# Kernel tuning notes

Measured on AMD Instinct MI355X. Metric: run time of the kernel, lower is better.

Reference implementation:

```python
import jax, jax.numpy as jnp
import numpy as np

B = 8
S_MAX = 1024
H = 12
HD = 64
D = H * HD
DFF = 4 * D
NEG = -1.0e9  # matches Triton kernel's -1000000000.0 mask value


def _layernorm(x, g, b, eps=1e-6):
    mu = jnp.mean(x, axis=-1, keepdims=True)
    var = jnp.mean((x - mu) ** 2, axis=-1, keepdims=True)
    return (x - mu) * jax.lax.rsqrt(var + eps) * g + b


def setup_inputs() -> dict:
    key = jax.random.key(0)
    ks = jax.random.split(key, 12)
    lengths = np.array([1024, 896, 768, 640, 896, 1024, 512, 384], dtype=np.int32)
    assert lengths.max() <= S_MAX and len(lengths) == B
    total = int(lengths.sum())  # 6144
    cu = jnp.asarray(np.concatenate([[0], np.cumsum(lengths)]), dtype=jnp.int32)
    s = 0.02
    return {
        "x": jax.random.normal(ks[0], (total, D), jnp.float32),
        "cu_seqlens": cu,
        "g1": jnp.ones((D,), jnp.float32),
        "beta1": jnp.zeros((D,), jnp.float32),
        "Wqkv": jax.random.normal(ks[1], (D, 3 * D), jnp.float32) * s,
        "bqkv": jnp.zeros((3 * D,), jnp.float32),
        "Wo": jax.random.normal(ks[2], (D, D), jnp.float32) * s,
        "bo": jnp.zeros((D,), jnp.float32),
        "g2": jnp.ones((D,), jnp.float32),
        "beta2": jnp.zeros((D,), jnp.float32),
        "W1": jax.random.normal(ks[3], (D, DFF), jnp.float32) * s,
        "b_fc1": jnp.zeros((DFF,), jnp.float32),
        "W2": jax.random.normal(ks[4], (DFF, D), jnp.float32) * s,
        "b_fc2": jnp.zeros((D,), jnp.float32),
    }


def _ragged_attention(q, k, v, cu_seqlens):
    # q,k,v: [Total, H, HD] packed ragged sequences; cu_seqlens: [B+1] int32
    total = q.shape[0]
    lens = cu_seqlens[1:] - cu_seqlens[:-1]                      # [B]
    s = jnp.arange(S_MAX)
    pad_idx = cu_seqlens[:-1, None] + jnp.minimum(s[None, :], lens[:, None] - 1)  # [B,S]
    valid = s[None, :] < lens[:, None]                           # [B,S]
    qp = q[pad_idx]                                              # [B,S,H,HD]
    kp = k[pad_idx]
    vp = v[pad_idx]
    scale = 1.0 / jnp.sqrt(jnp.float32(HD))
    scores = jnp.einsum("bqhd,bkhd->bhqk", qp, kp) * scale      # [B,H,S,S]
    scores = jnp.where(valid[:, None, None, :], scores, NEG)     # mask invalid keys
    p = jax.nn.softmax(scores, axis=-1)
    op = jnp.einsum("bhqk,bkhd->bqhd", p, vp)                   # [B,S,H,HD]
    # repack to [Total, H, HD]
    tok = jnp.arange(total)
    seg = jnp.searchsorted(cu_seqlens, tok, side="right") - 1    # sequence id per token
    pos = tok - cu_seqlens[seg]
    return op[seg, pos]


def _forward(x, cu_seqlens, g1, beta1, Wqkv, bqkv, Wo, bo, g2, beta2, W1, b_fc1, W2, b_fc2):
    total = x.shape[0]
    qkv = (_layernorm(x, g1, beta1) @ Wqkv + bqkv).reshape(total, 3, H, HD)
    q, k, v = qkv[:, 0], qkv[:, 1], qkv[:, 2]
    attn = _ragged_attention(q, k, v, cu_seqlens).reshape(total, D)
    x = x + (attn @ Wo + bo)                                     # proj_drop/ls1/drop_path identity (eval)
    h = _layernorm(x, g2, beta2)
    m = jax.nn.gelu(h @ W1 + b_fc1, approximate=False)
    return x + (m @ W2 + b_fc2)


def reference(x, cu_seqlens, g1, beta1, Wqkv, bqkv, Wo, bo, g2, beta2, W1, b_fc1, W2, b_fc2):
    return _forward(x, cu_seqlens, g1, beta1, Wqkv, bqkv, Wo, bo, g2, beta2, W1, b_fc1, W2, b_fc2)
```

## Files before the change

### kernel.cpp

```cpp
#include <hip/hip_runtime.h>
#include <hip/hip_bf16.h>
#include <stdint.h>
#include <string.h>

#define D_MODEL 768
#define H_HEADS 12
#define HD_ 64
#define N_QKV 2304

typedef __bf16 bf16x8 __attribute__((ext_vector_type(8)));
typedef float f32x4 __attribute__((ext_vector_type(4)));

__device__ __forceinline__ unsigned short f2bfbits(float f) {
  union { float f; unsigned u; } x; x.f = f;
  unsigned r = x.u + 0x7fffu + ((x.u >> 16) & 1u);
  return (unsigned short)(r >> 16);
}

__device__ __forceinline__ unsigned pk2(float a, float b) {
  union { float f; unsigned u; } x, y; x.f = a; y.f = b;
  return ((x.u + 0x8000u) >> 16) | ((y.u + 0x8000u) & 0xffff0000u);
}

#define FENCE_() __builtin_amdgcn_sched_barrier(0)
__device__ __forceinline__ void store_sync() {
  FENCE_();
  asm volatile("s_waitcnt lgkmcnt(0)");
  FENCE_();
  __builtin_amdgcn_s_barrier();
  FENCE_();
}

__global__ void transpose_w(const float* __restrict__ in, unsigned short* __restrict__ out,
                            int R, int C) {
  __shared__ float tile[32][33];
  int c0 = blockIdx.x * 32, r0 = blockIdx.y * 32;
  int tx = threadIdx.x, ty = threadIdx.y;
#pragma unroll
  for (int i = 0; i < 32; i += 8)
    tile[ty + i][tx] = in[(size_t)(r0 + ty + i) * C + c0 + tx];
  __syncthreads();
#pragma unroll
  for (int i = 0; i < 32; i += 8)
    out[(size_t)(c0 + ty + i) * R + r0 + tx] = f2bfbits(tile[tx][ty + i]);
}

__global__ void transpose_v(const unsigned short* __restrict__ qkv,
                            unsigned short* __restrict__ vT, int M) {
  __shared__ unsigned short tile[32][33];
  int t0 = blockIdx.x * 32, c0 = blockIdx.y * 32;
  int tx = threadIdx.x, ty = threadIdx.y;
#pragma unroll
  for (int i = 0; i < 32; i += 8)
    tile[ty + i][tx] = qkv[(size_t)(t0 + ty + i) * N_QKV + 1536 + c0 + tx];
  __syncthreads();
  int t = t0 + tx;
  int c = t & 63;
  int kp = ((c >> 5) << 5) | (((c >> 2) & 3) << 3) | (((c >> 4) & 1) << 2) | (c & 3);
  size_t col = (size_t)(t & ~63) + kp;
#pragma unroll
  for (int i = 0; i < 32; i += 8)
    vT[(size_t)(c0 + ty + i) * M + col] = tile[tx][ty + i];
}

__global__ void ln_bf16(const float* __restrict__ x, const float* __restrict__ g,
                        const float* __restrict__ be, unsigned short* __restrict__ out) {
  int row = blockIdx.x;
  const float* xr = x + (size_t)row * D_MODEL;
  int t = threadIdx.x;
  float v0 = xr[t], v1 = xr[t + 256], v2 = xr[t + 512];
  float s = v0 + v1 + v2;
  float s2 = v0 * v0 + v1 * v1 + v2 * v2;
#pragma unroll
  for (int off = 32; off > 0; off >>= 1) {
    s += __shfl_down(s, off, 64);
    s2 += __shfl_down(s2, off, 64);
  }
  __shared__ float red[8];
  int w = t >> 6, lane = t & 63;
  if (lane == 0) { red[w] = s; red[w + 4] = s2; }
  __syncthreads();
  if (t == 0) {
    float a = red[0] + red[1] + red[2] + red[3];
    float b = red[4] + red[5] + red[6] + red[7];
    red[0] = a * (1.0f / 768.0f);
    red[4] = b * (1.0f / 768.0f);
  }
  __syncthreads();
  float mu = red[0];
  float var = red[4] - mu * mu;
  float rs = rsqrtf(var + 1e-6f);
  unsigned short* orow = out + (size_t)row * D_MODEL;
  orow[t]       = f2bfbits((v0 - mu) * rs * g[t]       + be[t]);
  orow[t + 256] = f2bfbits((v1 - mu) * rs * g[t + 256] + be[t + 256]);
  orow[t + 512] = f2bfbits((v2 - mu) * rs * g[t + 512] + be[t + 512]);
}

template <int EPI>
__global__ void __launch_bounds__(256, 3)
gemm_rs(const unsigned short* __restrict__ A,
        const unsigned short* __restrict__ Bt,
        const float* __restrict__ bias,
        const float* __restrict__ res,
        void* __restrict__ outv,
        int M, int N, int K) {
  __shared__ unsigned short lA[2][128 * 32];
  __shared__ unsigned short lB[2][128 * 32];
  int tid = threadIdx.x;
  int w = tid >> 6, lane = tid & 63;
  int id = blockIdx.x;
  int nn = N >> 7, bandM = (M >> 7) >> 3;
  int xcd = id & 7, s = id >> 3;
  int mt = xcd * bandM + s / nn;
  int nt = s - (s / nn) * nn;
  int m0 = mt * 128, n0 = nt * 128;
  int wm = (w >> 1) * 64, wn = (w & 1) * 64;
  f32x4 acc[4][4];
#pragma unroll
  for (int i = 0; i < 4; i++)
#pragma unroll
    for (int j = 0; j < 4; j++) acc[i][j] = (f32x4){0.f, 0.f, 0.f, 0.f};

  int sr = tid >> 2, sc = tid & 3;
  const unsigned short* gA = A + (size_t)(m0 + sr) * K + sc * 8;
  const unsigned short* gB = Bt + (size_t)(n0 + sr) * K + sc * 8;
  int wOff = sr * 64 + ((((sr >> 1) & 3) ^ sc) * 16);
  int fm = lane & 15, fg = lane >> 4;

  uint4 pA0, pA1, pB0, pB1;
  uint4 qA0, qA1, qB0, qB1;

  int nk = K >> 5;
  pA0 = *(const uint4*)(gA);
  pA1 = *(const uint4*)(gA + (size_t)64 * K);
  pB0 = *(const uint4*)(gB);
  pB1 = *(const uint4*)(gB + (size_t)64 * K);
  qA0 = *(const uint4*)(gA + 32);
  qA1 = *(const uint4*)(gA + (size_t)64 * K + 32);
  qB0 = *(const uint4*)(gB + 32);
  qB1 = *(const uint4*)(gB + (size_t)64 * K + 32);

  for (int k = 0; k < nk; k += 2) {
    {
      char* la = (char*)&lA[0][0];
      char* lb = (char*)&lB[0][0];
      *(uint4*)(la + wOff) = pA0;
      *(uint4*)(la + wOff + 4096) = pA1;
      *(uint4*)(lb + wOff) = pB0;
      *(uint4*)(lb + wOff + 4096) = pB1;
      if (k + 2 < nk) {
        int k0 = (k + 2) * 32;
        pA0 = *(const uint4*)(gA + k0);
        pA1 = *(const uint4*)(gA + (size_t)64 * K + k0);
        pB0 = *(const uint4*)(gB + k0);
        pB1 = *(const uint4*)(gB + (size_t)64 * K + k0);
      }
      store_sync();
      bf16x8 af[4], bfr[4];
#pragma unroll
      for (int i = 0; i < 4; i++) {
        int rr = wm + i * 16 + fm;
        af[i] = *(const bf16x8*)(la + rr * 64 + ((((rr >> 1) & 3) ^ fg) * 16));
      }
#pragma unroll
      for (int j = 0; j < 4; j++) {
        int rr = wn + j * 16 + fm;
        bfr[j] = *(const bf16x8*)(lb + rr * 64 + ((((rr >> 1) & 3) ^ fg) * 16));
      }
#pragma unroll
      for (int i = 0; i < 4; i++)
#pragma unroll
        for (int j = 0; j < 4; j++)
          acc[i][j] = __builtin_amdgcn_mfma_f32_16x16x32_bf16(af[i], bfr[j], acc[i][j], 0, 0, 0);
      store_sync();
    }
    {
      char* la = (char*)&lA[1][0];
      char* lb = (char*)&lB[1][0];
      *(uint4*)(la + wOff) = qA0;
      *(uint4*)(la + wOff + 4096) = qA1;
      *(uint4*)(lb + wOff) = qB0;
      *(uint4*)(lb + wOff + 4096) = qB1;
      if (k + 3 < nk) {
        int k0 = (k + 3) * 32;
        qA0 = *(const uint4*)(gA + k0);
        qA1 = *(const uint4*)(gA + (size_t)64 * K + k0);
        qB0 = *(const uint4*)(gB + k0);
        qB1 = *(const uint4*)(gB + (size_t)64 * K + k0);
      }
      store_sync();
      bf16x8 af[4], bfr[4];
#pragma unroll
      for (int i = 0; i < 4; i++) {
        int rr = wm + i * 16 + fm;
        af[i] = *(const bf16x8*)(la + rr * 64 + ((((rr >> 1) & 3) ^ fg) * 16));
      }
#pragma unroll
      for (int j = 0; j < 4; j++) {
        int rr = wn + j * 16 + fm;
        bfr[j] = *(const bf16x8*)(lb + rr * 64 + ((((rr >> 1) & 3) ^ fg) * 16));
      }
#pragma unroll
      for (int i = 0; i < 4; i++)
#pragma unroll
        for (int j = 0; j < 4; j++)
          acc[i][j] = __builtin_amdgcn_mfma_f32_16x16x32_bf16(af[i], bfr[j], acc[i][j], 0, 0, 0);
      store_sync();
    }
  }

  int er = (lane >> 4) * 4, ec = lane & 15;
#pragma unroll
  for (int i = 0; i < 4; i++) {
#pragma unroll
    for (int j = 0; j < 4; j++) {
      int n = n0 + wn + j * 16 + ec;
      float bv = bias[n];
#pragma unroll
      for (int r = 0; r < 4; r++) {
        int m = m0 + wm + i * 16 + er + r;
        float v = acc[i][j][r] + bv;
        if (EPI == 1) {
          v += res[(size_t)m * N + n];
          ((float*)outv)[(size_t)m * N + n] = v;
        } else {
          if (EPI == 2) v = 0.5f * v * (1.0f + erff(v * 0.70710678118f));
          ((unsigned short*)outv)[(size_t)m * N + n] = f2bfbits(v);
        }
      }
    }
  }
}

template <int EPI>
__global__ void __launch_bounds__(256, 4)
gemm_n64(const unsigned short* __restrict__ A,
         const unsigned short* __restrict__ Bt,
         const float* __restrict__ bias,
         const float* __restrict__ res,
         void* __restrict__ outv,
         int M, int N, int K) {
  __shared__ unsigned short lA[2][128 * 32];
  __shared__ unsigned short lB[2][64 * 32];
  int tid = threadIdx.x;
  int w = tid >> 6, lane = tid & 63;
  int id = blockIdx.x;
  int nn = N >> 6, bandM = (M >> 7) >> 3;
  int xcd = id & 7, s = id >> 3;
  int mt = xcd * bandM + s / nn;
  int nt = s - (s / nn) * nn;
  int m0 = mt * 128, n0 = nt * 64;
  int wm = w * 32;
  f32x4 acc[2][4];
#pragma unroll
  for (int i = 0; i < 2; i++)
#pragma unroll
    for (int j = 0; j < 4; j++) acc[i][j] = (f32x4){0.f, 0.f, 0.f, 0.f};

  int sr = tid >> 2, sc = tid & 3;
  const unsigned short* gA = A + (size_t)(m0 + sr) * K + sc * 8;
  const unsigned short* gB = Bt + (size_t)(n0 + sr) * K + sc * 8;
  int wOff = sr * 64 + ((((sr >> 1) & 3) ^ sc) * 16);
  int fm = lane & 15, fg = lane >> 4;

  uint4 pA0, pA1, pB0;
  uint4 qA0, qA1, qB0;

  int nk = K >> 5;
  pA0 = *(const uint4*)(gA);
  pA1 = *(const uint4*)(gA + (size_t)64 * K);
  pB0 = *(const uint4*)(gB);
  qA0 = *(const uint4*)(gA + 32);
  qA1 = *(const uint4*)(gA + (size_t)64 * K + 32);
  qB0 = *(const uint4*)(gB + 32);

  for (int k = 0; k < nk; k += 2) {
    {
      char* la = (char*)&lA[0][0];
      char* lb = (char*)&lB[0][0];
      *(uint4*)(la + wOff) = pA0;
      *(uint4*)(la + wOff + 4096) = pA1;
      *(uint4*)(lb + wOff) = pB0;
      if (k + 2 < nk) {
        int k0 = (k + 2) * 32;
        pA0 = *(const uint4*)(gA + k0);
        pA1 = *(const uint4*)(gA + (size_t)64 * K + k0);
        pB0 = *(const uint4*)(gB + k0);
      }
      store_sync();
      bf16x8 af[2], bfr[4];
#pragma unroll
      for (int i = 0; i < 2; i++) {
        int rr = wm + i * 16 + fm;
        af[i] = *(const bf16x8*)(la + rr * 64 + ((((rr >> 1) & 3) ^ fg) * 16));
      }
#pragma unroll
      for (int j = 0; j < 4; j++) {
        int rr = j * 16 + fm;
        bfr[j] = *(const bf16x8*)(lb + rr * 64 + ((((rr >> 1) & 3) ^ fg) * 16));
      }
#pragma unroll
      for (int i = 0; i < 2; i++)
#pragma unroll
        for (int j = 0; j < 4; j++)
          acc[i][j] = __builtin_amdgcn_mfma_f32_16x16x32_bf16(af[i], bfr[j], acc[i][j], 0, 0, 0);
      store_sync();
    }
    {
      char* la = (char*)&lA[1][0];
      char* lb = (char*)&lB[1][0];
      *(uint4*)(la + wOff) = qA0;
      *(uint4*)(la + wOff + 4096) = qA1;
      *(uint4*)(lb + wOff) = qB0;
      if (k + 3 < nk) {
        int k0 = (k + 3) * 32;
        qA0 = *(const uint4*)(gA + k0);
        qA1 = *(const uint4*)(gA + (size_t)64 * K + k0);
        qB0 = *(const uint4*)(gB + k0);
      }
      store_sync();
      bf16x8 af[2], bfr[4];
#pragma unroll
      for (int i = 0; i < 2; i++) {
        int rr = wm + i * 16 + fm;
        af[i] = *(const bf16x8*)(la + rr * 64 + ((((rr >> 1) & 3) ^ fg) * 16));
      }
#pragma unroll
      for (int j = 0; j < 4; j++) {
        int rr = j * 16 + fm;
        bfr[j] = *(const bf16x8*)(lb + rr * 64 + ((((rr >> 1) & 3) ^ fg) * 16));
      }
#pragma unroll
      for (int i = 0; i < 2; i++)
#pragma unroll
        for (int j = 0; j < 4; j++)
          acc[i][j] = __builtin_amdgcn_mfma_f32_16x16x32_bf16(af[i], bfr[j], acc[i][j], 0, 0, 0);
      store_sync();
    }
  }

  int er = (lane >> 4) * 4, ec = lane & 15;
#pragma unroll
  for (int i = 0; i < 2; i++) {
#pragma unroll
    for (int j = 0; j < 4; j++) {
      int n = n0 + j * 16 + ec;
      float bv = bias[n];
#pragma unroll
      for (int r = 0; r < 4; r++) {
        int m = m0 + wm + i * 16 + er + r;
        float v = acc[i][j][r] + bv;
        if (EPI == 1) {
          v += res[(size_t)m * N + n];
          ((float*)outv)[(size_t)m * N + n] = v;
        } else {
          if (EPI == 2) v = 0.5f * v * (1.0f + erff(v * 0.70710678118f));
          ((unsigned short*)outv)[(size_t)m * N + n] = f2bfbits(v);
        }
      }
    }
  }
}

__global__ void attn_flash4(const unsigned short* __restrict__ qkv,
                            const unsigned short* __restrict__ vT,
                            const int* __restrict__ cu,
                            unsigned short* __restrict__ out, int M) {
  int id = blockIdx.x;
  int qc = id / 96;
  int bh = id - qc * 96;
  int b = bh / 12, h = bh - b * 12;
  int tok0 = cu[b];
  int len = cu[b + 1] - tok0;
  if (qc * 128 >= len) return;

  __shared__ unsigned short lK[2][64 * 64];
  __shared__ unsigned short lVT[2][64 * 64];

  int tid = threadIdx.x, w = tid >> 6, lane = tid & 63;
  int fm = lane & 15, fg = lane >> 4;
  int xm = fm & 7;
  int qbase = qc * 128 + w * 32;

  bf16x8 qf[2][2];
#pragma unroll
  for (int qs = 0; qs < 2; qs++)
#pragma unroll
    for (int kh = 0; kh < 2; kh++)
      qf[qs][kh] = *(const bf16x8*)(qkv + (size_t)(tok0 + qbase + qs * 16 + fm) * N_QKV +
                                    h * 64 + kh * 32 + fg * 8);

  f32x4 Oacc[2][4];
#pragma unroll
  for (int qs = 0; qs < 2; qs++)
#pragma unroll
    for (int dt = 0; dt < 4; dt++) Oacc[qs][dt] = (f32x4){0.f, 0.f, 0.f, 0.f};
  float lrow[2] = {0.f, 0.f};
  const float C2 = 0.18033688011112042f;

  int sr = tid >> 3, sp = tid & 7, sl = sp ^ (sr & 7);
  const unsigned short* kg0 = qkv + D_MODEL + h * 64 + sl * 8;
  const unsigned short* vg0 = vT + (size_t)(h * 64 + sr) * M + tok0 + sl * 8;

  uint4 rk0, rk1, rv0, rv1;
  auto gload = [&](int kt) {
    rk0 = *(const uint4*)(kg0 + (size_t)(tok0 + kt + sr) * N_QKV);
    rk1 = *(const uint4*)(kg0 + (size_t)(tok0 + kt + sr + 32) * N_QKV);
    rv0 = *(const uint4*)(vg0 + kt);
    rv1 = *(const uint4*)(vg0 + (size_t)32 * M + kt);
  };

  int nkt = len >> 6;
  gload(0);
  for (int kt = 0; kt < nkt; kt++) {
    int cur = kt & 1;
    *(uint4*)((char*)&lK[cur][0] + tid * 16) = rk0;
    *(uint4*)((char*)&lK[cur][0] + tid * 16 + 4096) = rk1;
    *(uint4*)((char*)&lVT[cur][0] + tid * 16) = rv0;
    *(uint4*)((char*)&lVT[cur][0] + tid * 16 + 4096) = rv1;
    if (kt + 1 < nkt) gload((kt + 1) * 64);
    store_sync();

    f32x4 s[2][4];
#pragma unroll
    for (int qs = 0; qs < 2; qs++)
#pragma unroll
      for (int t = 0; t < 4; t++) s[qs][t] = (f32x4){0.f, 0.f, 0.f, 0.f};
#pragma unroll
    for (int t = 0; t < 4; t++) {
      bf16x8 kf0 = *(const bf16x8*)&lK[cur][(t * 16 + fm) * 64 + ((fg ^ xm) * 8)];
      bf16x8 kf1 = *(const bf16x8*)&lK[cur][(t * 16 + fm) * 64 + (((4 + fg) ^ xm) * 8)];
#pragma unroll
      for (int qs = 0; qs < 2; qs++) {
        s[qs][t] = __builtin_amdgcn_mfma_f32_16x16x32_bf16(kf0, qf[qs][0], s[qs][t], 0, 0, 0);
        s[qs][t] = __builtin_amdgcn_mfma_f32_16x16x32_bf16(kf1, qf[qs][1], s[qs][t], 0, 0, 0);
      }
    }

    union { bf16x8 v; unsigned u[4]; } af[2][2];
#pragma unroll
    for (int qs = 0; qs < 2; qs++) {
      float ssum = 0.f;
#pragma unroll
      for (int t = 0; t < 4; t++) {
#pragma unroll
        for (int r = 0; r < 4; r++) {
          float p = exp2f(s[qs][t][r] * C2);
          s[qs][t][r] = p;
          ssum += p;
        }
      }
      lrow[qs] += ssum;
      af[qs][0].u[0] = pk2(s[qs][0][0], s[qs][0][1]);
      af[qs][0].u[1] = pk2(s[qs][0][2], s[qs][0][3]);
      af[qs][0].u[2] = pk2(s[qs][1][0], s[qs][1][1]);
      af[qs][0].u[3] = pk2(s[qs][1][2], s[qs][1][3]);
      af[qs][1].u[0] = pk2(s[qs][2][0], s[qs][2][1]);
      af[qs][1].u[1] = pk2(s[qs][2][2], s[qs][2][3]);
      af[qs][1].u[2] = pk2(s[qs][3][0], s[qs][3][1]);
      af[qs][1].u[3] = pk2(s[qs][3][2], s[qs][3][3]);
    }

#pragma unroll
    for (int dt = 0; dt < 4; dt++) {
      bf16x8 vf0 = *(const bf16x8*)&lVT[cur][(dt * 16 + fm) * 64 + ((fg ^ xm) * 8)];
      bf16x8 vf1 = *(const bf16x8*)&lVT[cur][(dt * 16 + fm) * 64 + (((4 + fg) ^ xm) * 8)];
#pragma unroll
      for (int qs = 0; qs < 2; qs++) {
        Oacc[qs][dt] = __builtin_amdgcn_mfma_f32_16x16x32_bf16(af[qs][0].v, vf0, Oacc[qs][dt], 0, 0, 0);
        Oacc[qs][dt] = __builtin_amdgcn_mfma_f32_16x16x32_bf16(af[qs][1].v, vf1, Oacc[qs][dt], 0, 0, 0);
      }
    }
  }

#pragma unroll
  for (int qs = 0; qs < 2; qs++) {
    lrow[qs] += __shfl_xor(lrow[qs], 16, 64);
    lrow[qs] += __shfl_xor(lrow[qs], 32, 64);
    float inv = 1.0f / lrow[qs];
    float ir[4];
#pragma unroll
    for (int r = 0; r < 4; r++) ir[r] = __shfl(inv, fg * 4 + r, 64);
#pragma unroll
    for (int dt = 0; dt < 4; dt++)
#pragma unroll
      for (int r = 0; r < 4; r++)
        out[(size_t)(tok0 + qbase + qs * 16 + fg * 4 + r) * D_MODEL + h * 64 + dt * 16 + fm] =
            f2bfbits(Oacc[qs][dt][r] * ir[r]);
  }
}

extern "C" void kernel_launch(void* const* d_in, const int* in_sizes, int n_in,
                              void* d_out, int out_size, void* d_ws, size_t ws_size,
                              hipStream_t stream) {
  const float* x    = (const float*)d_in[0];
  const int* cu     = (const int*)d_in[1];
  const float* g1   = (const float*)d_in[2];
  const float* be1  = (const float*)d_in[3];
  const float* Wqkv = (const float*)d_in[4];
  const float* bqkv = (const float*)d_in[5];
  const float* Wo   = (const float*)d_in[6];
  const float* bo   = (const float*)d_in[7];
  const float* g2   = (const float*)d_in[8];
  const float* be2  = (const float*)d_in[9];
  const float* W1   = (const float*)d_in[10];
  const float* bfc1 = (const float*)d_in[11];
  const float* W2   = (const float*)d_in[12];
  const float* bfc2 = (const float*)d_in[13];
  float* out = (float*)d_out;
  int M = in_sizes[0] / D_MODEL;

  unsigned short* WqkvT = (unsigned short*)d_ws;
  unsigned short* WoT   = WqkvT + 2304 * 768;
  unsigned short* W1T   = WoT + 768 * 768;
  unsigned short* W2T   = W1T + 3072 * 768;
  unsigned short* bufA  = W2T + 768 * 3072;
  float* x1             = (float*)(bufA + (size_t)M * D_MODEL);
  unsigned short* qkvb  = (unsigned short*)(x1 + (size_t)M * D_MODEL);
  unsigned short* vT = (unsigned short*)x1;

  dim3 b32(32, 8);
  transpose_w<<<dim3(2304 / 32, 768 / 32), b32, 0, stream>>>(Wqkv, WqkvT, 768, 2304);
  transpose_w<<<dim3(768 / 32, 768 / 32), b32, 0, stream>>>(Wo, WoT, 768, 768);
  transpose_w<<<dim3(3072 / 32, 768 / 32), b32, 0, stream>>>(W1, W1T, 768, 3072);
  transpose_w<<<dim3(768 / 32, 3072 / 32), b32, 0, stream>>>(W2, W2T, 3072, 768);

  ln_bf16<<<M, 256, 0, stream>>>(x, g1, be1, bufA);
  gemm_rs<0><<<(2304 / 128) * (M / 128), 256, 0, stream>>>(bufA, WqkvT, bqkv, nullptr, qkvb, M, 2304, 768);
  transpose_v<<<dim3(M / 32, 768 / 32), b32, 0, stream>>>(qkvb, vT, M);
  attn_flash4<<<8 * 96, 256, 0, stream>>>(qkvb, vT, cu, bufA, M);
  gemm_n64<1><<<(768 / 64) * (M / 128), 256, 0, stream>>>(bufA, WoT, bo, x, x1, M, 768, 768);
  ln_bf16<<<M, 256, 0, stream>>>(x1, g2, be2, bufA);
  gemm_rs<2><<<(3072 / 128) * (M / 128), 256, 0, stream>>>(bufA, W1T, bfc1, nullptr, qkvb, M, 3072, 768);
  gemm_n64<1><<<(768 / 64) * (M / 128), 256, 0, stream>>>(qkvb, W2T, bfc2, x1, out, M, 768, 3072);
}
```

Before: 343.3 us.

## Load GEMM A fragments directly from global memory, bypassing LDS staging

Both GEMM kernels now read the A-operand MFMA fragments straight from global memory into registers instead of staging A through double-buffered shared memory. Only B is staged in LDS, and the trailing barrier of each half-step is dropped because the double-buffered B tiles stay race-free with one barrier per stage. The aim is to cut LDS traffic, LDS footprint and barrier count. In exchange, A loads are issued in the same stage they are consumed with no register prefetch, so global-load latency may be exposed. Waves sharing the same A rows also fetch them redundantly from cache.

```diff
diff --git a/kernel.cpp b/kernel.cpp
--- a/kernel.cpp
+++ b/kernel.cpp
@@ -104,7 +104,6 @@
         const float* __restrict__ res,
         void* __restrict__ outv,
         int M, int N, int K) {
-  __shared__ unsigned short lA[2][128 * 32];
   __shared__ unsigned short lB[2][128 * 32];
   int tid = threadIdx.x;
   int w = tid >> 6, lane = tid & 63;
@@ -122,46 +121,34 @@
     for (int j = 0; j < 4; j++) acc[i][j] = (f32x4){0.f, 0.f, 0.f, 0.f};
 
   int sr = tid >> 2, sc = tid & 3;
-  const unsigned short* gA = A + (size_t)(m0 + sr) * K + sc * 8;
   const unsigned short* gB = Bt + (size_t)(n0 + sr) * K + sc * 8;
   int wOff = sr * 64 + ((((sr >> 1) & 3) ^ sc) * 16);
   int fm = lane & 15, fg = lane >> 4;
-
-  uint4 pA0, pA1, pB0, pB1;
-  uint4 qA0, qA1, qB0, qB1;
-
+  const unsigned short* gAf = A + (size_t)(m0 + wm + fm) * K + fg * 8;
+
+  uint4 pB0, pB1, qB0, qB1;
   int nk = K >> 5;
-  pA0 = *(const uint4*)(gA);
-  pA1 = *(const uint4*)(gA + (size_t)64 * K);
   pB0 = *(const uint4*)(gB);
   pB1 = *(const uint4*)(gB + (size_t)64 * K);
-  qA0 = *(const uint4*)(gA + 32);
-  qA1 = *(const uint4*)(gA + (size_t)64 * K + 32);
   qB0 = *(const uint4*)(gB + 32);
   qB1 = *(const uint4*)(gB + (size_t)64 * K + 32);
 
   for (int k = 0; k < nk; k += 2) {
     {
-      char* la = (char*)&lA[0][0];
       char* lb = (char*)&lB[0][0];
-      *(uint4*)(la + wOff) = pA0;
-      *(uint4*)(la + wOff + 4096) = pA1;
       *(uint4*)(lb + wOff) = pB0;
       *(uint4*)(lb + wOff + 4096) = pB1;
+      bf16x8 af[4];
+      const unsigned short* ga = gAf + k * 32;
+#pragma unroll
+      for (int i = 0; i < 4; i++) af[i] = *(const bf16x8*)(ga + (size_t)(i * 16) * K);
       if (k + 2 < nk) {
         int k0 = (k + 2) * 32;
-        pA0 = *(const uint4*)(gA + k0);
-        pA1 = *(const uint4*)(gA + (size_t)64 * K + k0);
         pB0 = *(const uint4*)(gB + k0);
         pB1 = *(const uint4*)(gB + (size_t)64 * K + k0);
       }
       store_sync();
-      bf16x8 af[4], bfr[4];
-#pragma unroll
-      for (int i = 0; i < 4; i++) {
-        int rr = wm + i * 16 + fm;
-        af[i] = *(const bf16x8*)(la + rr * 64 + ((((rr >> 1) & 3) ^ fg) * 16));
-      }
+      bf16x8 bfr[4];
 #pragma unroll
       for (int j = 0; j < 4; j++) {
         int rr = wn + j * 16 + fm;
@@ -172,29 +159,22 @@
 #pragma unroll
         for (int j = 0; j < 4; j++)
           acc[i][j] = __builtin_amdgcn_mfma_f32_16x16x32_bf16(af[i], bfr[j], acc[i][j], 0, 0, 0);
-      store_sync();
     }
     {
-      char* la = (char*)&lA[1][0];
       char* lb = (char*)&lB[1][0];
-      *(uint4*)(la + wOff) = qA0;
-      *(uint4*)(la + wOff + 4096) = qA1;
       *(uint4*)(lb + wOff) = qB0;
       *(uint4*)(lb + wOff + 4096) = qB1;
+      bf16x8 af[4];
+      const unsigned short* ga = gAf + (k + 1) * 32;
+#pragma unroll
+      for (int i = 0; i < 4; i++) af[i] = *(const bf16x8*)(ga + (size_t)(i * 16) * K);
       if (k + 3 < nk) {
         int k0 = (k + 3) * 32;
-        qA0 = *(const uint4*)(gA + k0);
-        qA1 = *(const uint4*)(gA + (size_t)64 * K + k0);
         qB0 = *(const uint4*)(gB + k0);
         qB1 = *(const uint4*)(gB + (size_t)64 * K + k0);
       }
       store_sync();
-      bf16x8 af[4], bfr[4];
-#pragma unroll
-      for (int i = 0; i < 4; i++) {
-        int rr = wm + i * 16 + fm;
-        af[i] = *(const bf16x8*)(la + rr * 64 + ((((rr >> 1) & 3) ^ fg) * 16));
-      }
+      bf16x8 bfr[4];
 #pragma unroll
       for (int j = 0; j < 4; j++) {
         int rr = wn + j * 16 + fm;
@@ -205,7 +185,6 @@
 #pragma unroll
         for (int j = 0; j < 4; j++)
           acc[i][j] = __builtin_amdgcn_mfma_f32_16x16x32_bf16(af[i], bfr[j], acc[i][j], 0, 0, 0);
-      store_sync();
     }
   }
 
@@ -240,7 +219,6 @@
          const float* __restrict__ res,
          void* __restrict__ outv,
          int M, int N, int K) {
-  __shared__ unsigned short lA[2][128 * 32];
   __shared__ unsigned short lB[2][64 * 32];
   int tid = threadIdx.x;
   int w = tid >> 6, lane = tid & 63;
@@ -258,42 +236,27 @@
     for (int j = 0; j < 4; j++) acc[i][j] = (f32x4){0.f, 0.f, 0.f, 0.f};
 
   int sr = tid >> 2, sc = tid & 3;
-  const unsigned short* gA = A + (size_t)(m0 + sr) * K + sc * 8;
   const unsigned short* gB = Bt + (size_t)(n0 + sr) * K + sc * 8;
   int wOff = sr * 64 + ((((sr >> 1) & 3) ^ sc) * 16);
   int fm = lane & 15, fg = lane >> 4;
-
-  uint4 pA0, pA1, pB0;
-  uint4 qA0, qA1, qB0;
-
+  const unsigned short* gAf = A + (size_t)(m0 + wm + fm) * K + fg * 8;
+
+  uint4 pB0, qB0;
   int nk = K >> 5;
-  pA0 = *(const uint4*)(gA);
-  pA1 = *(const uint4*)(gA + (size_t)64 * K);
   pB0 = *(const uint4*)(gB);
-  qA0 = *(const uint4*)(gA + 32);
-  qA1 = *(const uint4*)(gA + (size_t)64 * K + 32);
   qB0 = *(const uint4*)(gB + 32);
 
   for (int k = 0; k < nk; k += 2) {
     {
-      char* la = (char*)&lA[0][0];
       char* lb = (char*)&lB[0][0];
-      *(uint4*)(la + wOff) = pA0;
-      *(uint4*)(la + wOff + 4096) = pA1;
       *(uint4*)(lb + wOff) = pB0;
-      if (k + 2 < nk) {
-        int k0 = (k + 2) * 32;
-        pA0 = *(const uint4*)(gA + k0);
-        pA1 = *(const uint4*)(gA + (size_t)64 * K + k0);
-        pB0 = *(const uint4*)(gB + k0);
-      }
+      bf16x8 af[2];
+      const unsigned short* ga = gAf + k * 32;
+#pragma unroll
+      for (int i = 0; i < 2; i++) af[i] = *(const bf16x8*)(ga + (size_t)(i * 16) * K);
+      if (k + 2 < nk) pB0 = *(const uint4*)(gB + (k + 2) * 32);
       store_sync();
-      bf16x8 af[2], bfr[4];
-#pragma unroll
-      for (int i = 0; i < 2; i++) {
-        int rr = wm + i * 16 + fm;
-        af[i] = *(const bf16x8*)(la + rr * 64 + ((((rr >> 1) & 3) ^ fg) * 16));
-      }
+      bf16x8 bfr[4];
 #pragma unroll
       for (int j = 0; j < 4; j++) {
         int rr = j * 16 + fm;
@@ -304,27 +267,17 @@
 #pragma unroll
         for (int j = 0; j < 4; j++)
           acc[i][j] = __builtin_amdgcn_mfma_f32_16x16x32_bf16(af[i], bfr[j], acc[i][j], 0, 0, 0);
+    }
+    {
+      char* lb = (char*)&lB[1][0];
+      *(uint4*)(lb + wOff) = qB0;
+      bf16x8 af[2];
+      const unsigned short* ga = gAf + (k + 1) * 32;
+#pragma unroll
+      for (int i = 0; i < 2; i++) af[i] = *(const bf16x8*)(ga + (size_t)(i * 16) * K);
+      if (k + 3 < nk) qB0 = *(const uint4*)(gB + (k + 3) * 32);
       store_sync();
-    }
-    {
-      char* la = (char*)&lA[1][0];
-      char* lb = (char*)&lB[1][0];
-      *(uint4*)(la + wOff) = qA0;
-      *(uint4*)(la + wOff + 4096) = qA1;
-      *(uint4*)(lb + wOff) = qB0;
-      if (k + 3 < nk) {
-        int k0 = (k + 3) * 32;
-        qA0 = *(const uint4*)(gA + k0);
-        qA1 = *(const uint4*)(gA + (size_t)64 * K + k0);
-        qB0 = *(const uint4*)(gB + k0);
-      }
-      store_sync();
-      bf16x8 af[2], bfr[4];
-#pragma unroll
-      for (int i = 0; i < 2; i++) {
-        int rr = wm + i * 16 + fm;
-        af[i] = *(const bf16x8*)(la + rr * 64 + ((((rr >> 1) & 3) ^ fg) * 16));
-      }
+      bf16x8 bfr[4];
 #pragma unroll
       for (int j = 0; j < 4; j++) {
         int rr = j * 16 + fm;
@@ -335,7 +288,6 @@
 #pragma unroll
         for (int j = 0; j < 4; j++)
           acc[i][j] = __builtin_amdgcn_mfma_f32_16x16x32_bf16(af[i], bfr[j], acc[i][j], 0, 0, 0);
-      store_sync();
     }
   }
 
```

New measurement: 419.4 us. 1.22x slower.
